# Kernel optimization log

Hardware: AMD Instinct MI355X
Metric: run time of the kernel (lower is better)

The kernel has to match this reference:

```python
import jax, jax.numpy as jnp
import numpy as np

K = 3
PAD = 1
FS = 64  # feature_size == img_size for k=3, pad=1, stride=1
BN_EPS = 1e-5


def _unfold(x):
    # x: (B, C, H, W) -> (B, C*K*K, FS*FS), torch.nn.Unfold ordering (C-major, then kh, kw)
    B, C, H, W = x.shape
    xp = jnp.pad(x, ((0, 0), (0, 0), (PAD, PAD), (PAD, PAD)))
    patches = jnp.stack(
        [xp[:, :, i:i + FS, j:j + FS] for i in range(K) for j in range(K)],
        axis=2,
    )  # (B, C, K*K, FS, FS)
    return patches.reshape(B, C * K * K, FS * FS)


def setup_inputs() -> dict:
    key = jax.random.key(0)
    k1, k2, k3, k4, k5 = jax.random.split(key, 5)
    B, C, O = 32, 8, 32
    P = C * K * K  # 72
    return {
        "x": jax.random.normal(k1, (B, C, FS, FS), dtype=jnp.float32),
        "weight": jax.random.normal(k2, (1, O, P, FS * FS), dtype=jnp.float32) * 0.05,
        "bias": jax.random.normal(k3, (1, O, FS * FS), dtype=jnp.float32) * 0.05,
        "gamma": jax.random.uniform(k4, (O,), dtype=jnp.float32, minval=0.5, maxval=1.5),
        "beta": jax.random.normal(k5, (O,), dtype=jnp.float32) * 0.1,
    }


def reference(x, weight, bias, gamma, beta):
    B = x.shape[0]
    patches = _unfold(x)  # (B, P, F2)
    # per-pixel weights: (O, P, F2) contracted with patches over P
    y = jnp.einsum('opf,bpf->bof', weight[0], patches)  # (B, O, F2)
    y = y + bias  # (1, O, F2) broadcasts
    y = y.reshape(B, -1, FS, FS)
    # BatchNorm2d, training mode (biased batch variance)
    mean = jnp.mean(y, axis=(0, 2, 3), keepdims=True)
    var = jnp.mean(jnp.square(y - mean), axis=(0, 2, 3), keepdims=True)
    y = (y - mean) * jax.lax.rsqrt(var + BN_EPS)
    y = y * gamma[None, :, None, None] + beta[None, :, None, None]
    return y
```

## Files before the change

kernel.cpp:

```cpp
#include <hip/hip_runtime.h>

#define Oo    32
#define F2    4096
#define GRID  512
#define SLOTS 64
#define NTOT  (32 * F2)

typedef _Float16 h2 __attribute__((ext_vector_type(2)));
typedef _Float16 h8 __attribute__((ext_vector_type(8)));

#if __has_builtin(__builtin_amdgcn_fdot2)
#define DOT2(a, b, c) __builtin_amdgcn_fdot2((a), (b), (c), false)
#else
__device__ __forceinline__ float DOT2(h2 a, h2 b, float c) {
    return c + (float)a.x * (float)b.x + (float)a.y * (float)b.y;
}
#endif

__device__ __forceinline__ unsigned pkh2f(float a, float b) {
    h2 t; t.x = (_Float16)a; t.y = (_Float16)b;
    return __builtin_bit_cast(unsigned, t);
}
__device__ __forceinline__ h2 bch2(unsigned u) { return __builtin_bit_cast(h2, u); }

template <typename YT>
__global__ __launch_bounds__(512) void svconv_kernel(
    const float* __restrict__ x, const float* __restrict__ wgt,
    const float* __restrict__ bias, YT* __restrict__ y,
    float* __restrict__ psum, float* __restrict__ psumsq)
{
    __shared__ __align__(16) unsigned ldsX[3 * 32 * 68];
    __shared__ __align__(16) unsigned ldsW[2 * 9 * 4 * 64];

    const int tid = threadIdx.x;
    const int f   = tid & 63;
    const int bq  = tid >> 6;
    const int oq  = blockIdx.x >> 6;
    const int h   = blockIdx.x & 63;
    const int col = h * 64 + f;

    const bool wOK = (tid < 144);
    int wg = 0, wl = 0;
    {
        int s = wOK ? tid : 0;
        int o_ = s / 36, rm = s - 36 * o_;
        int k_ = rm >> 2, q_ = rm & 3;
        wg = ((oq * 4 + o_) * 72 + k_) * F2 + h * 64 + 16 * q_;
        wl = (k_ * 4 + o_) * 64 + 16 * q_;
    }

    bool xOK = false;
    int xg = 0, xl = 0;
    {
        int s = (tid < 384) ? tid : 0;
        int kh_ = s >> 7, b_ = (s >> 2) & 31, q_ = s & 3;
        int gh = h - 1 + kh_;
        xOK = (tid < 384) && ((unsigned)gh < 64u);
        xg = b_ * 32768 + gh * 64 + 16 * q_;
        xl = (kh_ * 32 + b_) * 68 + 16 * q_;
    }

    const int wi0 = (f == 0)  ? 64 : f - 1;
    const int wi2 = (f == 63) ? 65 : f + 1;

    float bz[4];
#pragma unroll
    for (int j = 0; j < 4; ++j) bz[j] = bias[(oq * 4 + j) * F2 + col];

    float acc[4][4];
#pragma unroll
    for (int j = 0; j < 4; ++j)
#pragma unroll
        for (int i = 0; i < 4; ++i) acc[j][i] = 0.f;

    float4 xr0[4], xr1[4], wr0[4], wr1[4];

    auto ISSUEX = [&](int cp) {
        if (xOK) {
            const int c0 = xg + cp * 8192;
#pragma unroll
            for (int e = 0; e < 4; ++e) {
                xr0[e] = *(const float4*)(x + c0 + 4 * e);
                xr1[e] = *(const float4*)(x + c0 + 4096 + 4 * e);
            }
        }
    };
    auto ISSUEW = [&](int cp) {
        if (wOK) {
            const int g0 = wg + cp * 18 * F2;
#pragma unroll
            for (int e = 0; e < 4; ++e) {
                wr0[e] = *(const float4*)(wgt + g0 + 4 * e);
                wr1[e] = *(const float4*)(wgt + g0 + 9 * F2 + 4 * e);
            }
        }
    };
    auto WRITEX = [&]() {
        if (xOK) {
#pragma unroll
            for (int e = 0; e < 4; ++e) {
                uint4 pk;
                pk.x = pkh2f(xr0[e].x, xr1[e].x);
                pk.y = pkh2f(xr0[e].y, xr1[e].y);
                pk.z = pkh2f(xr0[e].z, xr1[e].z);
                pk.w = pkh2f(xr0[e].w, xr1[e].w);
                *(uint4*)&ldsX[xl + 4 * e] = pk;
            }
        }
    };
    auto WRITEW = [&](int buf) {
        if (wOK) {
#pragma unroll
            for (int e = 0; e < 4; ++e) {
                uint4 pk;
                pk.x = pkh2f(wr0[e].x, wr1[e].x);
                pk.y = pkh2f(wr0[e].y, wr1[e].y);
                pk.z = pkh2f(wr0[e].z, wr1[e].z);
                pk.w = pkh2f(wr0[e].w, wr1[e].w);
                *(uint4*)&ldsW[buf * 2304 + wl + 4 * e] = pk;
            }
        }
    };
    auto COMPUTE = [&](int wbuf) {
        const unsigned* wb = &ldsW[wbuf * 2304];
#pragma unroll
        for (int k = 0; k < 9; ++k) {
            const int kh = k / 3, kw = k - 3 * kh;
            const int wi = (kw == 0) ? wi0 : ((kw == 1) ? f : wi2);
            h2 wv[4];
#pragma unroll
            for (int j = 0; j < 4; ++j) wv[j] = bch2(wb[k * 256 + j * 64 + f]);
#pragma unroll
            for (int i = 0; i < 4; ++i) {
                h2 xv = bch2(ldsX[(kh * 32 + bq * 4 + i) * 68 + wi]);
#pragma unroll
                for (int j = 0; j < 4; ++j)
                    acc[j][i] = DOT2(wv[j], xv, acc[j][i]);
            }
        }
    };

    ISSUEX(0); ISSUEW(0);
    for (int i = tid; i < 3 * 32 * 68; i += 512) ldsX[i] = 0u;
    __syncthreads();
    WRITEX(); WRITEW(0);
    __syncthreads();
    ISSUEX(1); ISSUEW(1);

#pragma unroll
    for (int cp = 0; cp < 4; ++cp) {
        COMPUTE(cp & 1);
        if (cp < 3) {
            __syncthreads();
            WRITEX(); WRITEW((cp + 1) & 1);
            __syncthreads();
            if (cp < 2) { ISSUEX(cp + 2); ISSUEW(cp + 2); }
        }
    }
    __syncthreads();

    float s_[4], ss_[4];
#pragma unroll
    for (int j = 0; j < 4; ++j) {
        s_[j] = 0.f; ss_[j] = 0.f;
#pragma unroll
        for (int i = 0; i < 4; ++i) {
            float a = acc[j][i] + bz[j];
            y[(size_t)((bq * 4 + i) * Oo + oq * 4 + j) * F2 + col] = (YT)a;
            s_[j] += a; ss_[j] = fmaf(a, a, ss_[j]);
        }
    }
    if (psum != nullptr) {
#pragma unroll
        for (int j = 0; j < 4; ++j)
#pragma unroll
            for (int d = 32; d >= 1; d >>= 1) {
                s_[j]  += __shfl_down(s_[j],  d, 64);
                ss_[j] += __shfl_down(ss_[j], d, 64);
            }
        float* scr = (float*)ldsX;
        if (f == 0) {
#pragma unroll
            for (int j = 0; j < 4; ++j) {
                scr[bq * 4 + j]      = s_[j];
                scr[32 + bq * 4 + j] = ss_[j];
            }
        }
        __syncthreads();
        if (tid < 32) {
            int j = tid >> 3, g = tid & 7;
            float v  = scr[g * 4 + j];
            float vv = scr[32 + g * 4 + j];
#pragma unroll
            for (int d = 4; d >= 1; d >>= 1) {
                v  += __shfl_down(v,  d, 8);
                vv += __shfl_down(vv, d, 8);
            }
            if (g == 0) {
                psum[(oq * 4 + j) * SLOTS + h]   = v;
                psumsq[(oq * 4 + j) * SLOTS + h] = vv;
            }
        }
    }
}

__global__ __launch_bounds__(256) void bnapply_fused_kernel(
    const _Float16* __restrict__ yh, const float* __restrict__ psum,
    const float* __restrict__ psumsq, const float* __restrict__ gamma,
    const float* __restrict__ beta, float* __restrict__ y)
{
    __shared__ float scsh[2];
    const int o = (blockIdx.x >> 1) & 31;
    const int t = threadIdx.x;
    if (t < 64) {
        float v  = psum[o * SLOTS + t];
        float vv = psumsq[o * SLOTS + t];
#pragma unroll
        for (int d = 32; d >= 1; d >>= 1) {
            v  += __shfl_down(v,  d, 64);
            vv += __shfl_down(vv, d, 64);
        }
        if (t == 0) {
            float mean = v / (float)NTOT;
            float var  = vv / (float)NTOT - mean * mean;
            float rstd = rsqrtf(var + 1e-5f);
            float scl  = gamma[o] * rstd;
            scsh[0] = scl;
            scsh[1] = beta[o] - mean * scl;
        }
    }
    __syncthreads();
    const float scl = scsh[0], sh = scsh[1];

    int i = blockIdx.x * 256 + t;
    h8 v = ((const h8*)yh)[i];
    float4 lo, hi;
    lo.x = fmaf((float)v[0], scl, sh);
    lo.y = fmaf((float)v[1], scl, sh);
    lo.z = fmaf((float)v[2], scl, sh);
    lo.w = fmaf((float)v[3], scl, sh);
    hi.x = fmaf((float)v[4], scl, sh);
    hi.y = fmaf((float)v[5], scl, sh);
    hi.z = fmaf((float)v[6], scl, sh);
    hi.w = fmaf((float)v[7], scl, sh);
    ((float4*)y)[2 * i]     = lo;
    ((float4*)y)[2 * i + 1] = hi;
}

__global__ __launch_bounds__(64) void bnstats_kernel(
    const float* __restrict__ psum, const float* __restrict__ psumsq,
    const float* __restrict__ gamma, const float* __restrict__ beta,
    float* __restrict__ scsh)
{
    const int o = blockIdx.x;
    const int t = threadIdx.x;
    float s  = psum[o * SLOTS + t];
    float ss = psumsq[o * SLOTS + t];
#pragma unroll
    for (int d = 32; d >= 1; d >>= 1) {
        s  += __shfl_down(s, d, 64);
        ss += __shfl_down(ss, d, 64);
    }
    if (t == 0) {
        float mean = s / (float)NTOT;
        float var  = ss / (float)NTOT - mean * mean;
        float rstd = rsqrtf(var + 1e-5f);
        float scl  = gamma[o] * rstd;
        scsh[o]      = scl;
        scsh[Oo + o] = beta[o] - mean * scl;
    }
}

__global__ __launch_bounds__(256) void bnapply_kernel(
    float* __restrict__ y, const float* __restrict__ scsh)
{
    int i = blockIdx.x * 256 + threadIdx.x;
    float4 v = ((const float4*)y)[i];
    int o = (i >> 10) & 31;
    float scl = scsh[o], sh = scsh[Oo + o];
    v.x = fmaf(v.x, scl, sh);
    v.y = fmaf(v.y, scl, sh);
    v.z = fmaf(v.z, scl, sh);
    v.w = fmaf(v.w, scl, sh);
    ((float4*)y)[i] = v;
}

__global__ __launch_bounds__(256) void bnreduce_y_kernel(
    const float* __restrict__ y, float* __restrict__ seg, float* __restrict__ segsq)
{
    const int o  = blockIdx.x >> 3;
    const int sg = blockIdx.x & 7;
    const int t  = threadIdx.x;
    float s = 0.f, ss = 0.f;
    for (int i = t; i < 4 * 1024; i += 256) {
        int b   = sg * 4 + (i >> 10);
        int fof = (i & 1023) * 4;
        float4 v = *(const float4*)(y + (size_t)(b * Oo + o) * F2 + fof);
        s  += (v.x + v.y) + (v.z + v.w);
        ss += v.x * v.x + v.y * v.y + v.z * v.z + v.w * v.w;
    }
#pragma unroll
    for (int d = 32; d >= 1; d >>= 1) {
        s  += __shfl_down(s, d, 64);
        ss += __shfl_down(ss, d, 64);
    }
    __shared__ float ls[4], lss[4];
    int wv = t >> 6, ln = t & 63;
    if (ln == 0) { ls[wv] = s; lss[wv] = ss; }
    __syncthreads();
    if (t == 0) {
        seg[blockIdx.x]   = (ls[0] + ls[1]) + (ls[2] + ls[3]);
        segsq[blockIdx.x] = (lss[0] + lss[1]) + (lss[2] + lss[3]);
    }
}

__global__ __launch_bounds__(256) void bnstats2_kernel(
    const float* __restrict__ seg, const float* __restrict__ segsq,
    const float* __restrict__ gamma, const float* __restrict__ beta,
    float* __restrict__ scsh)
{
    const int t = threadIdx.x;
    const int o = t >> 3, g = t & 7;
    float v  = seg[t];
    float vv = segsq[t];
#pragma unroll
    for (int d = 4; d >= 1; d >>= 1) {
        v  += __shfl_down(v,  d, 8);
        vv += __shfl_down(vv, d, 8);
    }
    if (g == 0) {
        float mean = v / (float)NTOT;
        float var  = vv / (float)NTOT - mean * mean;
        float rstd = rsqrtf(var + 1e-5f);
        float scl  = gamma[o] * rstd;
        scsh[o]      = scl;
        scsh[Oo + o] = beta[o] - mean * scl;
    }
}

extern "C" void kernel_launch(void* const* d_in, const int* in_sizes, int n_in,
                              void* d_out, int out_size, void* d_ws, size_t ws_size,
                              hipStream_t stream)
{
    const float* x     = (const float*)d_in[0];
    const float* wgt   = (const float*)d_in[1];
    const float* bias  = (const float*)d_in[2];
    const float* gamma = (const float*)d_in[3];
    const float* beta  = (const float*)d_in[4];
    float* y = (float*)d_out;

    const size_t n_elems    = (size_t)NTOT * Oo;
    const size_t yh_bytes   = n_elems * sizeof(_Float16);
    const size_t psum_bytes = (size_t)(2 * Oo * SLOTS + 2 * Oo) * sizeof(float);

    if (ws_size >= yh_bytes + psum_bytes) {
        _Float16* yh  = (_Float16*)d_ws;
        float* psum   = (float*)((char*)d_ws + yh_bytes);
        float* psumsq = psum + Oo * SLOTS;
        svconv_kernel<_Float16><<<GRID, 512, 0, stream>>>(x, wgt, bias, yh, psum, psumsq);
        bnapply_fused_kernel<<<(int)(n_elems / 8 / 256), 256, 0, stream>>>(
            yh, psum, psumsq, gamma, beta, y);
    } else if (ws_size >= psum_bytes) {
        float* psum   = (float*)d_ws;
        float* psumsq = psum + Oo * SLOTS;
        float* scsh   = psumsq + Oo * SLOTS;
        svconv_kernel<float><<<GRID, 512, 0, stream>>>(x, wgt, bias, y, psum, psumsq);
        bnstats_kernel<<<Oo, 64, 0, stream>>>(psum, psumsq, gamma, beta, scsh);
        bnapply_kernel<<<(int)(n_elems / 4 / 256), 256, 0, stream>>>(y, scsh);
    } else {
        float* seg   = (float*)d_ws;
        float* segsq = seg + 256;
        float* scsh  = segsq + 256;
        svconv_kernel<float><<<GRID, 512, 0, stream>>>(x, wgt, bias, y, nullptr, nullptr);
        bnreduce_y_kernel<<<256, 256, 0, stream>>>(y, seg, segsq);
        bnstats2_kernel<<<1, 256, 0, stream>>>(seg, segsq, gamma, beta, scsh);
        bnapply_kernel<<<(int)(n_elems / 4 / 256), 256, 0, stream>>>(y, scsh);
    }
}
```

Before: 30.13 us.

## Compute two output rows per block to reuse loaded input halo rows

Each block now processes two adjacent image rows instead of one, halving the grid to 256 blocks and loading four input rows (instead of three per single row) into LDS. This shares the halo rows between the two outputs, so less input is loaded per output. The load mapping is redistributed across all 512 threads, and the BN partial-sum slots shrink from 64 to 32 per channel. In exchange each thread holds twice as many accumulators, which adds register pressure, and the smaller grid may leave compute units idle on a large GPU.

```diff
diff --git a/kernel.cpp b/kernel.cpp
--- a/kernel.cpp
+++ b/kernel.cpp
@@ -2,8 +2,8 @@
 
 #define Oo    32
 #define F2    4096
-#define GRID  512
-#define SLOTS 64
+#define GRID  256
+#define SLOTS 32
 #define NTOT  (32 * F2)
 
 typedef _Float16 h2 __attribute__((ext_vector_type(2)));
@@ -29,119 +29,133 @@
     const float* __restrict__ bias, YT* __restrict__ y,
     float* __restrict__ psum, float* __restrict__ psumsq)
 {
-    __shared__ __align__(16) unsigned ldsX[3 * 32 * 68];
-    __shared__ __align__(16) unsigned ldsW[2 * 9 * 4 * 64];
+    __shared__ __align__(16) unsigned ldsX[4 * 32 * 68];
+    __shared__ __align__(16) unsigned ldsW[2 * 9 * 4 * 128];
 
     const int tid = threadIdx.x;
     const int f   = tid & 63;
     const int bq  = tid >> 6;
-    const int oq  = blockIdx.x >> 6;
-    const int h   = blockIdx.x & 63;
-    const int col = h * 64 + f;
-
-    const bool wOK = (tid < 144);
-    int wg = 0, wl = 0;
-    {
-        int s = wOK ? tid : 0;
-        int o_ = s / 36, rm = s - 36 * o_;
-        int k_ = rm >> 2, q_ = rm & 3;
-        wg = ((oq * 4 + o_) * 72 + k_) * F2 + h * 64 + 16 * q_;
-        wl = (k_ * 4 + o_) * 64 + 16 * q_;
-    }
-
-    bool xOK = false;
-    int xg = 0, xl = 0;
-    {
-        int s = (tid < 384) ? tid : 0;
-        int kh_ = s >> 7, b_ = (s >> 2) & 31, q_ = s & 3;
-        int gh = h - 1 + kh_;
-        xOK = (tid < 384) && ((unsigned)gh < 64u);
-        xg = b_ * 32768 + gh * 64 + 16 * q_;
-        xl = (kh_ * 32 + b_) * 68 + 16 * q_;
+    const int oq  = blockIdx.x >> 5;
+    const int hh  = blockIdx.x & 31;
+    const int h0  = 2 * hh;
+
+    bool wOKm[3];
+    int  wg[3], wl[3];
+#pragma unroll
+    for (int m = 0; m < 3; ++m) {
+        int s = tid + m * 512;
+        wOKm[m] = (s < 1152);
+        if (!wOKm[m]) s = 0;
+        int o_ = s / 288, rm = s - 288 * o_;
+        int k_ = rm >> 5, q_ = rm & 31;
+        wg[m] = ((oq * 4 + o_) * 72 + k_) * F2 + hh * 128 + 4 * q_;
+        wl[m] = (k_ * 4 + o_) * 128 + 4 * q_;
+    }
+
+    bool xOKm[4];
+    int  xg[4], xl[4];
+#pragma unroll
+    for (int m = 0; m < 4; ++m) {
+        int s = tid + m * 512;
+        int b_ = s >> 6, rm = s & 63;
+        int khr = rm >> 4, q = rm & 15;
+        int gh = h0 - 1 + khr;
+        xOKm[m] = ((unsigned)gh < 64u);
+        xg[m] = b_ * 32768 + gh * 64 + 4 * q;
+        xl[m] = (khr * 32 + b_) * 68 + 4 * q;
     }
 
     const int wi0 = (f == 0)  ? 64 : f - 1;
     const int wi2 = (f == 63) ? 65 : f + 1;
 
-    float bz[4];
-#pragma unroll
-    for (int j = 0; j < 4; ++j) bz[j] = bias[(oq * 4 + j) * F2 + col];
-
-    float acc[4][4];
+    float bz[4][2];
 #pragma unroll
     for (int j = 0; j < 4; ++j)
 #pragma unroll
-        for (int i = 0; i < 4; ++i) acc[j][i] = 0.f;
-
-    float4 xr0[4], xr1[4], wr0[4], wr1[4];
+        for (int r = 0; r < 2; ++r)
+            bz[j][r] = bias[(oq * 4 + j) * F2 + (h0 + r) * 64 + f];
+
+    float acc[4][2][4];
+#pragma unroll
+    for (int j = 0; j < 4; ++j)
+#pragma unroll
+        for (int r = 0; r < 2; ++r)
+#pragma unroll
+            for (int i = 0; i < 4; ++i) acc[j][r][i] = 0.f;
+
+    float4 xr0[4], xr1[4], wr0[3], wr1[3];
 
     auto ISSUEX = [&](int cp) {
-        if (xOK) {
-            const int c0 = xg + cp * 8192;
-#pragma unroll
-            for (int e = 0; e < 4; ++e) {
-                xr0[e] = *(const float4*)(x + c0 + 4 * e);
-                xr1[e] = *(const float4*)(x + c0 + 4096 + 4 * e);
+        const int co = cp * 8192;
+#pragma unroll
+        for (int m = 0; m < 4; ++m) {
+            if (xOKm[m]) {
+                xr0[m] = *(const float4*)(x + xg[m] + co);
+                xr1[m] = *(const float4*)(x + xg[m] + co + 4096);
+            } else {
+                xr0[m] = make_float4(0.f, 0.f, 0.f, 0.f);
+                xr1[m] = xr0[m];
             }
         }
     };
     auto ISSUEW = [&](int cp) {
-        if (wOK) {
-            const int g0 = wg + cp * 18 * F2;
-#pragma unroll
-            for (int e = 0; e < 4; ++e) {
-                wr0[e] = *(const float4*)(wgt + g0 + 4 * e);
-                wr1[e] = *(const float4*)(wgt + g0 + 9 * F2 + 4 * e);
-            }
-        }
+        const int off = cp * 18 * F2;
+#pragma unroll
+        for (int m = 0; m < 3; ++m)
+            if (wOKm[m]) {
+                wr0[m] = *(const float4*)(wgt + wg[m] + off);
+                wr1[m] = *(const float4*)(wgt + wg[m] + off + 9 * F2);
+            }
     };
     auto WRITEX = [&]() {
-        if (xOK) {
-#pragma unroll
-            for (int e = 0; e < 4; ++e) {
+#pragma unroll
+        for (int m = 0; m < 4; ++m) {
+            uint4 pk;
+            pk.x = pkh2f(xr0[m].x, xr1[m].x);
+            pk.y = pkh2f(xr0[m].y, xr1[m].y);
+            pk.z = pkh2f(xr0[m].z, xr1[m].z);
+            pk.w = pkh2f(xr0[m].w, xr1[m].w);
+            *(uint4*)&ldsX[xl[m]] = pk;
+        }
+    };
+    auto WRITEW = [&](int buf) {
+#pragma unroll
+        for (int m = 0; m < 3; ++m)
+            if (wOKm[m]) {
                 uint4 pk;
-                pk.x = pkh2f(xr0[e].x, xr1[e].x);
-                pk.y = pkh2f(xr0[e].y, xr1[e].y);
-                pk.z = pkh2f(xr0[e].z, xr1[e].z);
-                pk.w = pkh2f(xr0[e].w, xr1[e].w);
-                *(uint4*)&ldsX[xl + 4 * e] = pk;
-            }
-        }
-    };
-    auto WRITEW = [&](int buf) {
-        if (wOK) {
-#pragma unroll
-            for (int e = 0; e < 4; ++e) {
-                uint4 pk;
-                pk.x = pkh2f(wr0[e].x, wr1[e].x);
-                pk.y = pkh2f(wr0[e].y, wr1[e].y);
-                pk.z = pkh2f(wr0[e].z, wr1[e].z);
-                pk.w = pkh2f(wr0[e].w, wr1[e].w);
-                *(uint4*)&ldsW[buf * 2304 + wl + 4 * e] = pk;
-            }
-        }
+                pk.x = pkh2f(wr0[m].x, wr1[m].x);
+                pk.y = pkh2f(wr0[m].y, wr1[m].y);
+                pk.z = pkh2f(wr0[m].z, wr1[m].z);
+                pk.w = pkh2f(wr0[m].w, wr1[m].w);
+                *(uint4*)&ldsW[buf * 4608 + wl[m]] = pk;
+            }
     };
     auto COMPUTE = [&](int wbuf) {
-        const unsigned* wb = &ldsW[wbuf * 2304];
+        const unsigned* wb = &ldsW[wbuf * 4608];
 #pragma unroll
         for (int k = 0; k < 9; ++k) {
             const int kh = k / 3, kw = k - 3 * kh;
             const int wi = (kw == 0) ? wi0 : ((kw == 1) ? f : wi2);
-            h2 wv[4];
-#pragma unroll
-            for (int j = 0; j < 4; ++j) wv[j] = bch2(wb[k * 256 + j * 64 + f]);
-#pragma unroll
-            for (int i = 0; i < 4; ++i) {
-                h2 xv = bch2(ldsX[(kh * 32 + bq * 4 + i) * 68 + wi]);
-#pragma unroll
-                for (int j = 0; j < 4; ++j)
-                    acc[j][i] = DOT2(wv[j], xv, acc[j][i]);
-            }
+            h2 wv[4][2];
+#pragma unroll
+            for (int j = 0; j < 4; ++j)
+#pragma unroll
+                for (int r = 0; r < 2; ++r)
+                    wv[j][r] = bch2(wb[(k * 4 + j) * 128 + r * 64 + f]);
+#pragma unroll
+            for (int r = 0; r < 2; ++r)
+#pragma unroll
+                for (int i = 0; i < 4; ++i) {
+                    h2 xv = bch2(ldsX[((kh + r) * 32 + bq * 4 + i) * 68 + wi]);
+#pragma unroll
+                    for (int j = 0; j < 4; ++j)
+                        acc[j][r][i] = DOT2(wv[j][r], xv, acc[j][r][i]);
+                }
         }
     };
 
     ISSUEX(0); ISSUEW(0);
-    for (int i = tid; i < 3 * 32 * 68; i += 512) ldsX[i] = 0u;
+    for (int i = tid; i < 4 * 32 * 68; i += 512) ldsX[i] = 0u;
     __syncthreads();
     WRITEX(); WRITEW(0);
     __syncthreads();
@@ -161,15 +175,19 @@
 
     float s_[4], ss_[4];
 #pragma unroll
-    for (int j = 0; j < 4; ++j) {
-        s_[j] = 0.f; ss_[j] = 0.f;
-#pragma unroll
-        for (int i = 0; i < 4; ++i) {
-            float a = acc[j][i] + bz[j];
-            y[(size_t)((bq * 4 + i) * Oo + oq * 4 + j) * F2 + col] = (YT)a;
-            s_[j] += a; ss_[j] = fmaf(a, a, ss_[j]);
-        }
-    }
+    for (int j = 0; j < 4; ++j) { s_[j] = 0.f; ss_[j] = 0.f; }
+#pragma unroll
+    for (int j = 0; j < 4; ++j)
+#pragma unroll
+        for (int r = 0; r < 2; ++r) {
+            const int col = (h0 + r) * 64 + f;
+#pragma unroll
+            for (int i = 0; i < 4; ++i) {
+                float a = acc[j][r][i] + bz[j][r];
+                y[(size_t)((bq * 4 + i) * Oo + oq * 4 + j) * F2 + col] = (YT)a;
+                s_[j] += a; ss_[j] = fmaf(a, a, ss_[j]);
+            }
+        }
     if (psum != nullptr) {
 #pragma unroll
         for (int j = 0; j < 4; ++j)
@@ -197,8 +215,8 @@
                 vv += __shfl_down(vv, d, 8);
             }
             if (g == 0) {
-                psum[(oq * 4 + j) * SLOTS + h]   = v;
-                psumsq[(oq * 4 + j) * SLOTS + h] = vv;
+                psum[(oq * 4 + j) * SLOTS + hh]   = v;
+                psumsq[(oq * 4 + j) * SLOTS + hh] = vv;
             }
         }
     }
@@ -212,13 +230,13 @@
     __shared__ float scsh[2];
     const int o = (blockIdx.x >> 1) & 31;
     const int t = threadIdx.x;
-    if (t < 64) {
+    if (t < 32) {
         float v  = psum[o * SLOTS + t];
         float vv = psumsq[o * SLOTS + t];
 #pragma unroll
-        for (int d = 32; d >= 1; d >>= 1) {
-            v  += __shfl_down(v,  d, 64);
-            vv += __shfl_down(vv, d, 64);
+        for (int d = 16; d >= 1; d >>= 1) {
+            v  += __shfl_down(v,  d, 32);
+            vv += __shfl_down(vv, d, 32);
         }
         if (t == 0) {
             float mean = v / (float)NTOT;
@@ -254,8 +272,8 @@
 {
     const int o = blockIdx.x;
     const int t = threadIdx.x;
-    float s  = psum[o * SLOTS + t];
-    float ss = psumsq[o * SLOTS + t];
+    float s = 0.f, ss = 0.f;
+    if (t < SLOTS) { s = psum[o * SLOTS + t]; ss = psumsq[o * SLOTS + t]; }
 #pragma unroll
     for (int d = 32; d >= 1; d >>= 1) {
         s  += __shfl_down(s, d, 64);
```

Measured after the change: 38.03 us. 1.26x slower.
